# Kernel optimization log

Measured on AMD Instinct MI355X. Metric: run time of the kernel, lower is better.

The kernel has to match this reference:

```python
import jax, jax.numpy as jnp
import numpy as np

SEQ_LEN = 512
PRED_LEN = 96
N_BINS = 5


def setup_inputs() -> dict:
    key = jax.random.key(0)
    k1, k2, k3 = jax.random.split(key, 3)
    x = jax.random.normal(k1, (64, 1024, SEQ_LEN), dtype=jnp.float32)
    # nn.Linear(seq_len, pred_len): weight (pred_len, seq_len), bias (pred_len,)
    W = jax.random.normal(k2, (PRED_LEN, SEQ_LEN), dtype=jnp.float32) / np.sqrt(SEQ_LEN)
    b = jax.random.normal(k3, (PRED_LEN,), dtype=jnp.float32) * 0.01
    return {"x": x, "W": W, "b": b}


def reference(x, W, b):
    # Exact low-pass trend: keep lowest N_BINS rfft bins, zero the rest, invert.
    X = jnp.fft.rfft(x, axis=-1)                      # (B, N, seq_len//2+1) complex
    n_freq = X.shape[-1]
    keep = (jnp.arange(n_freq) < N_BINS)              # low-pass mask
    X_low = jnp.where(keep, X, 0.0)
    trend = jnp.fft.irfft(X_low, n=SEQ_LEN, axis=-1).astype(x.dtype)  # (B, N, seq_len)
    resid = x - trend
    trend_forecast = jnp.einsum('bns,ps->bnp', trend, W) + b          # (B, N, pred_len)
    return (trend_forecast, resid)
```

## Files before the change

kernel.cpp:

```cpp
#include <hip/hip_runtime.h>

#define SEQL 512
#define PREDL 96
#define NB 9
#define WBPAD 12
#define RU 8

typedef float fvec4 __attribute__((ext_vector_type(4)));

__device__ __forceinline__ float wave_sum_bcast(float v) {
    int t;
    t = __builtin_amdgcn_update_dpp(0, __float_as_int(v), 0x111, 0xf, 0xf, true); v += __int_as_float(t);
    t = __builtin_amdgcn_update_dpp(0, __float_as_int(v), 0x112, 0xf, 0xf, true); v += __int_as_float(t);
    t = __builtin_amdgcn_update_dpp(0, __float_as_int(v), 0x114, 0xf, 0xf, true); v += __int_as_float(t);
    t = __builtin_amdgcn_update_dpp(0, __float_as_int(v), 0x118, 0xf, 0xf, true); v += __int_as_float(t);
    t = __builtin_amdgcn_update_dpp(0, __float_as_int(v), 0x142, 0xf, 0xf, true); v += __int_as_float(t);
    t = __builtin_amdgcn_update_dpp(0, __float_as_int(v), 0x143, 0xf, 0xf, true); v += __int_as_float(t);
    return __int_as_float(__builtin_amdgcn_readlane(__float_as_int(v), 63));
}

__global__ void basis_kernel(float* __restrict__ tbl) {
    int s = threadIdx.x;
    if (s >= SEQL) return;
    tbl[0 * SEQL + s] = 1.0f;
    #pragma unroll
    for (int k = 1; k <= 4; ++k) {
        int m = (k * s) & (SEQL - 1);
        float ang = (float)m * (6.283185307179586f / SEQL);
        float sn, cs;
        __sincosf(ang, &sn, &cs);
        tbl[(2 * k - 1) * SEQL + s] = cs;
        tbl[(2 * k    ) * SEQL + s] = sn;
    }
}

__global__ __launch_bounds__(64)
void wb_kernel(const float* __restrict__ W, const float* __restrict__ tbl,
               float* __restrict__ wb) {
    int p = blockIdx.x;
    int lane = threadIdx.x;
    const float* wr = W + (size_t)p * SEQL + lane * 8;
    float4 wa = *(const float4*)(wr);
    float4 wz = *(const float4*)(wr + 4);
    float wv[8] = {wa.x, wa.y, wa.z, wa.w, wz.x, wz.y, wz.z, wz.w};
    #pragma unroll
    for (int j = 0; j < NB; ++j) {
        const float* bj = tbl + j * SEQL + lane * 8;
        float4 b0 = *(const float4*)bj;
        float4 b1 = *(const float4*)(bj + 4);
        float bb[8] = {b0.x, b0.y, b0.z, b0.w, b1.x, b1.y, b1.z, b1.w};
        float acc = 0.f;
        #pragma unroll
        for (int e = 0; e < 8; ++e) acc += wv[e] * bb[e];
        float s = wave_sum_bcast(acc);
        if (lane == 0) wb[p * WBPAD + j] = s;
    }
}

__global__ __launch_bounds__(256, 2)
void detrend_kernel(const float* __restrict__ x, const float* __restrict__ bias,
                    const float* __restrict__ tbl, const float* __restrict__ wb,
                    float* __restrict__ fc, float* __restrict__ resid, int nrows) {
    const int lane = threadIdx.x & 63;
    const int wid  = threadIdx.x >> 6;
    const int gw   = blockIdx.x * (blockDim.x >> 6) + wid;
    const int r0   = gw * RU;
    if (r0 >= nrows) return;

    float4 xl[RU][2];
    #pragma unroll
    for (int u = 0; u < RU; ++u) {
        const float* xr = x + (size_t)(r0 + u) * SEQL + lane * 8;
        xl[u][0] = *(const float4*)xr;
        xl[u][1] = *(const float4*)(xr + 4);
    }

    float bas[NB][8];
    #pragma unroll
    for (int j = 0; j < NB; ++j) {
        const float* bj = tbl + j * SEQL + lane * 8;
        float4 b0 = *(const float4*)bj;
        float4 b1 = *(const float4*)(bj + 4);
        bas[j][0] = b0.x; bas[j][1] = b0.y; bas[j][2] = b0.z; bas[j][3] = b0.w;
        bas[j][4] = b1.x; bas[j][5] = b1.y; bas[j][6] = b1.z; bas[j][7] = b1.w;
    }
    const int p0 = lane;
    const int p1 = 64 + lane;
    float wb0[NB], wb1[NB], bv0, bv1 = 0.f;
    #pragma unroll
    for (int j = 0; j < NB; ++j) wb0[j] = wb[p0 * WBPAD + j];
    bv0 = bias[p0];
    if (lane < 32) {
        #pragma unroll
        for (int j = 0; j < NB; ++j) wb1[j] = wb[p1 * WBPAD + j];
        bv1 = bias[p1];
    }

    #pragma unroll
    for (int u = 0; u < RU; ++u) {
        float xv[8] = {xl[u][0].x, xl[u][0].y, xl[u][0].z, xl[u][0].w,
                       xl[u][1].x, xl[u][1].y, xl[u][1].z, xl[u][1].w};
        float acc[NB];
        #pragma unroll
        for (int j = 0; j < NB; ++j) acc[j] = 0.f;
        #pragma unroll
        for (int e = 0; e < 8; ++e)
            #pragma unroll
            for (int j = 0; j < NB; ++j) acc[j] += xv[e] * bas[j][e];
        acc[0] *= (1.0f / SEQL);
        #pragma unroll
        for (int j = 1; j < NB; ++j) acc[j] *= (2.0f / SEQL);
        float c[NB];
        #pragma unroll
        for (int j = 0; j < NB; ++j) c[j] = wave_sum_bcast(acc[j]);

        float rv[8];
        #pragma unroll
        for (int e = 0; e < 8; ++e) {
            float t = 0.f;
            #pragma unroll
            for (int j = 0; j < NB; ++j) t += c[j] * bas[j][e];
            rv[e] = xv[e] - t;
        }
        float* rr = resid + (size_t)(r0 + u) * SEQL + lane * 8;
        fvec4 v0 = {rv[0], rv[1], rv[2], rv[3]};
        fvec4 v1 = {rv[4], rv[5], rv[6], rv[7]};
        __builtin_nontemporal_store(v0, (fvec4*)rr);
        __builtin_nontemporal_store(v1, (fvec4*)(rr + 4));

        float* fr = fc + (size_t)(r0 + u) * PREDL;
        float f0 = bv0;
        #pragma unroll
        for (int j = 0; j < NB; ++j) f0 += c[j] * wb0[j];
        __builtin_nontemporal_store(f0, fr + p0);
        if (lane < 32) {
            float f1 = bv1;
            #pragma unroll
            for (int j = 0; j < NB; ++j) f1 += c[j] * wb1[j];
            __builtin_nontemporal_store(f1, fr + p1);
        }
    }
}

extern "C" void kernel_launch(void* const* d_in, const int* in_sizes, int n_in,
                              void* d_out, int out_size, void* d_ws, size_t ws_size,
                              hipStream_t stream) {
    const float* x = (const float*)d_in[0];
    const float* W = (const float*)d_in[1];
    const float* b = (const float*)d_in[2];
    float* fc = (float*)d_out;
    const int nrows = in_sizes[0] / SEQL;
    float* resid = fc + (size_t)nrows * PREDL;
    float* tbl = (float*)d_ws;
    float* wb  = tbl + NB * SEQL;

    hipLaunchKernelGGL(basis_kernel, dim3(1), dim3(SEQL), 0, stream, tbl);
    hipLaunchKernelGGL(wb_kernel, dim3(PREDL), dim3(64), 0, stream, W, tbl, wb);
    hipLaunchKernelGGL(detrend_kernel, dim3(2048), dim3(256), 0, stream,
                       x, b, tbl, wb, fc, resid, nrows);
}
```

Baseline: 67.83 us.

## Split detrend into coefficient pass and apply pass with grid-stride loops

Splits the fused detrend kernel into two kernels. The first computes the 9 Fourier coefficients per row and writes them to a workspace buffer. The second re-reads x together with those coefficients to produce the residual and the forecast. Both use persistent grid-stride loops, and the fused fallback also becomes grid-stride with smaller unrolling. This is meant to separate the reduction-heavy phase from the store-heavy phase, at the cost of reading x twice, which adds about 128 MB of extra traffic.

Result: slower. 99.56 us (+46.8%).

```diff
diff --git a/kernel.cpp b/kernel.cpp
--- a/kernel.cpp
+++ b/kernel.cpp
@@ -4,7 +4,9 @@
 #define PREDL 96
 #define NB 9
 #define WBPAD 12
-#define RU 8
+#define RU1 8
+#define RU2 4
+#define RUF 4
 
 typedef float fvec4 __attribute__((ext_vector_type(4)));
 
@@ -57,23 +59,143 @@
     }
 }
 
-__global__ __launch_bounds__(256, 2)
+__global__ __launch_bounds__(256)
+void coef_kernel(const float* __restrict__ x, const float* __restrict__ tbl,
+                 float* __restrict__ cbuf, int nrows) {
+    const int lane = threadIdx.x & 63;
+    const int wid  = threadIdx.x >> 6;
+    const int gw   = blockIdx.x * (blockDim.x >> 6) + wid;
+    const int nw   = gridDim.x * (blockDim.x >> 6);
+
+    float bas[NB][8];
+    #pragma unroll
+    for (int j = 0; j < NB; ++j) {
+        const float* bj = tbl + j * SEQL + lane * 8;
+        float4 b0 = *(const float4*)bj;
+        float4 b1 = *(const float4*)(bj + 4);
+        bas[j][0] = b0.x; bas[j][1] = b0.y; bas[j][2] = b0.z; bas[j][3] = b0.w;
+        bas[j][4] = b1.x; bas[j][5] = b1.y; bas[j][6] = b1.z; bas[j][7] = b1.w;
+    }
+
+    for (int r0 = gw * RU1; r0 < nrows; r0 += nw * RU1) {
+        float4 xl[RU1][2];
+        #pragma unroll
+        for (int u = 0; u < RU1; ++u) {
+            const float* xr = x + (size_t)(r0 + u) * SEQL + lane * 8;
+            xl[u][0] = *(const float4*)xr;
+            xl[u][1] = *(const float4*)(xr + 4);
+        }
+        #pragma unroll
+        for (int u = 0; u < RU1; ++u) {
+            float xv[8] = {xl[u][0].x, xl[u][0].y, xl[u][0].z, xl[u][0].w,
+                           xl[u][1].x, xl[u][1].y, xl[u][1].z, xl[u][1].w};
+            float acc[NB];
+            #pragma unroll
+            for (int j = 0; j < NB; ++j) acc[j] = 0.f;
+            #pragma unroll
+            for (int e = 0; e < 8; ++e)
+                #pragma unroll
+                for (int j = 0; j < NB; ++j) acc[j] += xv[e] * bas[j][e];
+            acc[0] *= (1.0f / SEQL);
+            #pragma unroll
+            for (int j = 1; j < NB; ++j) acc[j] *= (2.0f / SEQL);
+            float c[NB];
+            #pragma unroll
+            for (int j = 0; j < NB; ++j) c[j] = wave_sum_bcast(acc[j]);
+            float v = c[0];
+            #pragma unroll
+            for (int j = 1; j < NB; ++j) v = (lane == j) ? c[j] : v;
+            if (lane < NB) cbuf[(size_t)(r0 + u) * NB + lane] = v;
+        }
+    }
+}
+
+__global__ __launch_bounds__(256)
+void apply_kernel(const float* __restrict__ x, const float* __restrict__ bias,
+                  const float* __restrict__ tbl, const float* __restrict__ wb,
+                  const float* __restrict__ cbuf,
+                  float* __restrict__ fc, float* __restrict__ resid, int nrows) {
+    const int lane = threadIdx.x & 63;
+    const int wid  = threadIdx.x >> 6;
+    const int gw   = blockIdx.x * (blockDim.x >> 6) + wid;
+    const int nw   = gridDim.x * (blockDim.x >> 6);
+
+    float bas[NB][8];
+    #pragma unroll
+    for (int j = 0; j < NB; ++j) {
+        const float* bj = tbl + j * SEQL + lane * 8;
+        float4 b0 = *(const float4*)bj;
+        float4 b1 = *(const float4*)(bj + 4);
+        bas[j][0] = b0.x; bas[j][1] = b0.y; bas[j][2] = b0.z; bas[j][3] = b0.w;
+        bas[j][4] = b1.x; bas[j][5] = b1.y; bas[j][6] = b1.z; bas[j][7] = b1.w;
+    }
+    const int p0 = lane;
+    const int p1 = 64 + lane;
+    float wb0[NB], wb1[NB], bv0, bv1 = 0.f;
+    #pragma unroll
+    for (int j = 0; j < NB; ++j) wb0[j] = wb[p0 * WBPAD + j];
+    bv0 = bias[p0];
+    if (lane < 32) {
+        #pragma unroll
+        for (int j = 0; j < NB; ++j) wb1[j] = wb[p1 * WBPAD + j];
+        bv1 = bias[p1];
+    }
+
+    for (int r0 = gw * RU2; r0 < nrows; r0 += nw * RU2) {
+        float4 xl[RU2][2];
+        #pragma unroll
+        for (int u = 0; u < RU2; ++u) {
+            const float* xr = x + (size_t)(r0 + u) * SEQL + lane * 8;
+            xl[u][0] = *(const float4*)xr;
+            xl[u][1] = *(const float4*)(xr + 4);
+        }
+        float cmy = (lane < RU2 * NB) ? cbuf[(size_t)r0 * NB + lane] : 0.f;
+
+        #pragma unroll
+        for (int u = 0; u < RU2; ++u) {
+            float c[NB];
+            #pragma unroll
+            for (int j = 0; j < NB; ++j) c[j] = __shfl(cmy, u * NB + j, 64);
+
+            float xv[8] = {xl[u][0].x, xl[u][0].y, xl[u][0].z, xl[u][0].w,
+                           xl[u][1].x, xl[u][1].y, xl[u][1].z, xl[u][1].w};
+            float rv[8];
+            #pragma unroll
+            for (int e = 0; e < 8; ++e) {
+                float t = 0.f;
+                #pragma unroll
+                for (int j = 0; j < NB; ++j) t += c[j] * bas[j][e];
+                rv[e] = xv[e] - t;
+            }
+            float* rr = resid + (size_t)(r0 + u) * SEQL + lane * 8;
+            fvec4 v0 = {rv[0], rv[1], rv[2], rv[3]};
+            fvec4 v1 = {rv[4], rv[5], rv[6], rv[7]};
+            __builtin_nontemporal_store(v0, (fvec4*)rr);
+            __builtin_nontemporal_store(v1, (fvec4*)(rr + 4));
+
+            float* fr = fc + (size_t)(r0 + u) * PREDL;
+            float f0 = bv0;
+            #pragma unroll
+            for (int j = 0; j < NB; ++j) f0 += c[j] * wb0[j];
+            __builtin_nontemporal_store(f0, fr + p0);
+            if (lane < 32) {
+                float f1 = bv1;
+                #pragma unroll
+                for (int j = 0; j < NB; ++j) f1 += c[j] * wb1[j];
+                __builtin_nontemporal_store(f1, fr + p1);
+            }
+        }
+    }
+}
+
+__global__ __launch_bounds__(256)
 void detrend_kernel(const float* __restrict__ x, const float* __restrict__ bias,
                     const float* __restrict__ tbl, const float* __restrict__ wb,
                     float* __restrict__ fc, float* __restrict__ resid, int nrows) {
     const int lane = threadIdx.x & 63;
     const int wid  = threadIdx.x >> 6;
     const int gw   = blockIdx.x * (blockDim.x >> 6) + wid;
-    const int r0   = gw * RU;
-    if (r0 >= nrows) return;
-
-    float4 xl[RU][2];
-    #pragma unroll
-    for (int u = 0; u < RU; ++u) {
-        const float* xr = x + (size_t)(r0 + u) * SEQL + lane * 8;
-        xl[u][0] = *(const float4*)xr;
-        xl[u][1] = *(const float4*)(xr + 4);
-    }
+    const int nw   = gridDim.x * (blockDim.x >> 6);
 
     float bas[NB][8];
     #pragma unroll
@@ -96,48 +218,57 @@
         bv1 = bias[p1];
     }
 
-    #pragma unroll
-    for (int u = 0; u < RU; ++u) {
-        float xv[8] = {xl[u][0].x, xl[u][0].y, xl[u][0].z, xl[u][0].w,
-                       xl[u][1].x, xl[u][1].y, xl[u][1].z, xl[u][1].w};
-        float acc[NB];
-        #pragma unroll
-        for (int j = 0; j < NB; ++j) acc[j] = 0.f;
-        #pragma unroll
-        for (int e = 0; e < 8; ++e)
-            #pragma unroll
-            for (int j = 0; j < NB; ++j) acc[j] += xv[e] * bas[j][e];
-        acc[0] *= (1.0f / SEQL);
-        #pragma unroll
-        for (int j = 1; j < NB; ++j) acc[j] *= (2.0f / SEQL);
-        float c[NB];
-        #pragma unroll
-        for (int j = 0; j < NB; ++j) c[j] = wave_sum_bcast(acc[j]);
-
-        float rv[8];
-        #pragma unroll
-        for (int e = 0; e < 8; ++e) {
-            float t = 0.f;
-            #pragma unroll
-            for (int j = 0; j < NB; ++j) t += c[j] * bas[j][e];
-            rv[e] = xv[e] - t;
-        }
-        float* rr = resid + (size_t)(r0 + u) * SEQL + lane * 8;
-        fvec4 v0 = {rv[0], rv[1], rv[2], rv[3]};
-        fvec4 v1 = {rv[4], rv[5], rv[6], rv[7]};
-        __builtin_nontemporal_store(v0, (fvec4*)rr);
-        __builtin_nontemporal_store(v1, (fvec4*)(rr + 4));
-
-        float* fr = fc + (size_t)(r0 + u) * PREDL;
-        float f0 = bv0;
-        #pragma unroll
-        for (int j = 0; j < NB; ++j) f0 += c[j] * wb0[j];
-        __builtin_nontemporal_store(f0, fr + p0);
-        if (lane < 32) {
-            float f1 = bv1;
-            #pragma unroll
-            for (int j = 0; j < NB; ++j) f1 += c[j] * wb1[j];
-            __builtin_nontemporal_store(f1, fr + p1);
+    for (int r0 = gw * RUF; r0 < nrows; r0 += nw * RUF) {
+        float4 xl[RUF][2];
+        #pragma unroll
+        for (int u = 0; u < RUF; ++u) {
+            const float* xr = x + (size_t)(r0 + u) * SEQL + lane * 8;
+            xl[u][0] = *(const float4*)xr;
+            xl[u][1] = *(const float4*)(xr + 4);
+        }
+        #pragma unroll
+        for (int u = 0; u < RUF; ++u) {
+            float xv[8] = {xl[u][0].x, xl[u][0].y, xl[u][0].z, xl[u][0].w,
+                           xl[u][1].x, xl[u][1].y, xl[u][1].z, xl[u][1].w};
+            float acc[NB];
+            #pragma unroll
+            for (int j = 0; j < NB; ++j) acc[j] = 0.f;
+            #pragma unroll
+            for (int e = 0; e < 8; ++e)
+                #pragma unroll
+                for (int j = 0; j < NB; ++j) acc[j] += xv[e] * bas[j][e];
+            acc[0] *= (1.0f / SEQL);
+            #pragma unroll
+            for (int j = 1; j < NB; ++j) acc[j] *= (2.0f / SEQL);
+            float c[NB];
+            #pragma unroll
+            for (int j = 0; j < NB; ++j) c[j] = wave_sum_bcast(acc[j]);
+
+            float rv[8];
+            #pragma unroll
+            for (int e = 0; e < 8; ++e) {
+                float t = 0.f;
+                #pragma unroll
+                for (int j = 0; j < NB; ++j) t += c[j] * bas[j][e];
+                rv[e] = xv[e] - t;
+            }
+            float* rr = resid + (size_t)(r0 + u) * SEQL + lane * 8;
+            fvec4 v0 = {rv[0], rv[1], rv[2], rv[3]};
+            fvec4 v1 = {rv[4], rv[5], rv[6], rv[7]};
+            __builtin_nontemporal_store(v0, (fvec4*)rr);
+            __builtin_nontemporal_store(v1, (fvec4*)(rr + 4));
+
+            float* fr = fc + (size_t)(r0 + u) * PREDL;
+            float f0 = bv0;
+            #pragma unroll
+            for (int j = 0; j < NB; ++j) f0 += c[j] * wb0[j];
+            __builtin_nontemporal_store(f0, fr + p0);
+            if (lane < 32) {
+                float f1 = bv1;
+                #pragma unroll
+                for (int j = 0; j < NB; ++j) f1 += c[j] * wb1[j];
+                __builtin_nontemporal_store(f1, fr + p1);
+            }
         }
     }
 }
@@ -153,9 +284,19 @@
     float* resid = fc + (size_t)nrows * PREDL;
     float* tbl = (float*)d_ws;
     float* wb  = tbl + NB * SEQL;
+    float* cbuf = wb + PREDL * WBPAD;
+    const size_t ws_need = ((size_t)NB * SEQL + PREDL * WBPAD + (size_t)nrows * NB) * 4;
 
     hipLaunchKernelGGL(basis_kernel, dim3(1), dim3(SEQL), 0, stream, tbl);
     hipLaunchKernelGGL(wb_kernel, dim3(PREDL), dim3(64), 0, stream, W, tbl, wb);
-    hipLaunchKernelGGL(detrend_kernel, dim3(2048), dim3(256), 0, stream,
-                       x, b, tbl, wb, fc, resid, nrows);
-}
+
+    if (ws_size >= ws_need) {
+        hipLaunchKernelGGL(coef_kernel, dim3(1024), dim3(256), 0, stream,
+                           x, tbl, cbuf, nrows);
+        hipLaunchKernelGGL(apply_kernel, dim3(1024), dim3(256), 0, stream,
+                           x, b, tbl, wb, cbuf, fc, resid, nrows);
+    } else {
+        hipLaunchKernelGGL(detrend_kernel, dim3(2048), dim3(256), 0, stream,
+                           x, b, tbl, wb, fc, resid, nrows);
+    }
+}
```

## Persistent double-buffered detrend loop with half-period symmetry basis folding

Applied to the files above, without the earlier changes.

Turns the detrend kernel into a grid-stride persistent loop over half as many blocks, prefetching the next group of rows into a second register buffer while the current group is processed. Each lane now reads elements s and s+256 and uses the parity of the low-frequency basis under a half-period shift, so it keeps only half the basis table in registers and does roughly half the projection multiplies. Rows per step drop from 8 to 4 and the occupancy hint in the launch bounds is removed. The aim is to overlap memory loads with the reduction work and to cut register pressure and ALU work, but the deeper loop logic and fewer blocks may leave bandwidth unused.

Result: faster. 60.47 us (-10.8%).

```diff
diff --git a/kernel.cpp b/kernel.cpp
--- a/kernel.cpp
+++ b/kernel.cpp
@@ -4,7 +4,7 @@
 #define PREDL 96
 #define NB 9
 #define WBPAD 12
-#define RU 8
+#define RU 4
 
 typedef float fvec4 __attribute__((ext_vector_type(4)));
 
@@ -57,32 +57,21 @@
     }
 }
 
-__global__ __launch_bounds__(256, 2)
+__global__ __launch_bounds__(256)
 void detrend_kernel(const float* __restrict__ x, const float* __restrict__ bias,
                     const float* __restrict__ tbl, const float* __restrict__ wb,
                     float* __restrict__ fc, float* __restrict__ resid, int nrows) {
     const int lane = threadIdx.x & 63;
     const int wid  = threadIdx.x >> 6;
     const int gw   = blockIdx.x * (blockDim.x >> 6) + wid;
-    const int r0   = gw * RU;
-    if (r0 >= nrows) return;
-
-    float4 xl[RU][2];
-    #pragma unroll
-    for (int u = 0; u < RU; ++u) {
-        const float* xr = x + (size_t)(r0 + u) * SEQL + lane * 8;
-        xl[u][0] = *(const float4*)xr;
-        xl[u][1] = *(const float4*)(xr + 4);
-    }
-
-    float bas[NB][8];
-    #pragma unroll
-    for (int j = 0; j < NB; ++j) {
-        const float* bj = tbl + j * SEQL + lane * 8;
-        float4 b0 = *(const float4*)bj;
-        float4 b1 = *(const float4*)(bj + 4);
+    const int nw   = gridDim.x * (blockDim.x >> 6);
+    const int step = nw * RU;
+
+    float bas[NB][4];
+    #pragma unroll
+    for (int j = 1; j < NB; ++j) {
+        float4 b0 = *(const float4*)(tbl + j * SEQL + lane * 4);
         bas[j][0] = b0.x; bas[j][1] = b0.y; bas[j][2] = b0.z; bas[j][3] = b0.w;
-        bas[j][4] = b1.x; bas[j][5] = b1.y; bas[j][6] = b1.z; bas[j][7] = b1.w;
     }
     const int p0 = lane;
     const int p1 = 64 + lane;
@@ -96,50 +85,103 @@
         bv1 = bias[p1];
     }
 
+    float4 bufA0[RU], bufA1[RU];
+    float4 bufB0[RU], bufB1[RU];
+
+    int r = gw * RU;
+    if (r >= nrows) return;
+
     #pragma unroll
     for (int u = 0; u < RU; ++u) {
-        float xv[8] = {xl[u][0].x, xl[u][0].y, xl[u][0].z, xl[u][0].w,
-                       xl[u][1].x, xl[u][1].y, xl[u][1].z, xl[u][1].w};
-        float acc[NB];
-        #pragma unroll
-        for (int j = 0; j < NB; ++j) acc[j] = 0.f;
-        #pragma unroll
-        for (int e = 0; e < 8; ++e)
+        const float* xr = x + (size_t)(r + u) * SEQL + lane * 4;
+        bufA0[u] = *(const float4*)xr;
+        bufB0[u] = *(const float4*)(xr + 256);
+    }
+
+    #define PROCESS(BA, BB, RR)                                                     \
+    {                                                                               \
+        _Pragma("unroll")                                                           \
+        for (int u = 0; u < RU; ++u) {                                              \
+            float ue[4], ve[4];                                                     \
+            ue[0]=BA[u].x+BB[u].x; ue[1]=BA[u].y+BB[u].y;                           \
+            ue[2]=BA[u].z+BB[u].z; ue[3]=BA[u].w+BB[u].w;                           \
+            ve[0]=BA[u].x-BB[u].x; ve[1]=BA[u].y-BB[u].y;                           \
+            ve[2]=BA[u].z-BB[u].z; ve[3]=BA[u].w-BB[u].w;                           \
+            float acc[NB];                                                          \
+            acc[0] = (ue[0]+ue[1]) + (ue[2]+ue[3]);                                 \
+            acc[1]=0.f; acc[2]=0.f; acc[5]=0.f; acc[6]=0.f;       \
+            acc[3]=0.f; acc[4]=0.f; acc[7]=0.f; acc[8]=0.f;      \
+            _Pragma("unroll")                                                       \
+            for (int e = 0; e < 4; ++e) {                                           \
+                acc[1] += ve[e]*bas[1][e]; acc[2] += ve[e]*bas[2][e];               \
+                acc[5] += ve[e]*bas[5][e]; acc[6] += ve[e]*bas[6][e];               \
+                acc[3] += ue[e]*bas[3][e]; acc[4] += ue[e]*bas[4][e];               \
+                acc[7] += ue[e]*bas[7][e]; acc[8] += ue[e]*bas[8][e];               \
+            }                                                                       \
+            acc[0] *= (1.0f / SEQL);                                                \
+            _Pragma("unroll")                                                       \
+            for (int j = 1; j < NB; ++j) acc[j] *= (2.0f / SEQL);                   \
+            float c[NB];                                                            \
+            _Pragma("unroll")                                                       \
+            for (int j = 0; j < NB; ++j) c[j] = wave_sum_bcast(acc[j]);             \
+            float r0v[4], r1v[4];                                                   \
+            _Pragma("unroll")                                                       \
+            for (int e = 0; e < 4; ++e) {                                           \
+                float te = c[0] + c[3]*bas[3][e] + c[4]*bas[4][e]                   \
+                                + c[7]*bas[7][e] + c[8]*bas[8][e];                  \
+                float to = c[1]*bas[1][e] + c[2]*bas[2][e]                          \
+                         + c[5]*bas[5][e] + c[6]*bas[6][e];                         \
+                float av = (e==0)?BA[u].x:(e==1)?BA[u].y:(e==2)?BA[u].z:BA[u].w;    \
+                float bv = (e==0)?BB[u].x:(e==1)?BB[u].y:(e==2)?BB[u].z:BB[u].w;    \
+                r0v[e] = av - (te + to);                                            \
+                r1v[e] = bv - (te - to);                                            \
+            }                                                                       \
+            float* rr = resid + (size_t)((RR) + u) * SEQL + lane * 4;               \
+            fvec4 s0v = {r0v[0], r0v[1], r0v[2], r0v[3]};                           \
+            fvec4 s1v = {r1v[0], r1v[1], r1v[2], r1v[3]};                           \
+            __builtin_nontemporal_store(s0v, (fvec4*)rr);                           \
+            __builtin_nontemporal_store(s1v, (fvec4*)(rr + 256));                   \
+            float* fr = fc + (size_t)((RR) + u) * PREDL;                            \
+            float f0 = bv0;                                                         \
+            _Pragma("unroll")                                                       \
+            for (int j = 0; j < NB; ++j) f0 += c[j] * wb0[j];                       \
+            __builtin_nontemporal_store(f0, fr + p0);                               \
+            if (lane < 32) {                                                        \
+                float f1 = bv1;                                                     \
+                _Pragma("unroll")                                                   \
+                for (int j = 0; j < NB; ++j) f1 += c[j] * wb1[j];                   \
+                __builtin_nontemporal_store(f1, fr + p1);                           \
+            }                                                                       \
+        }                                                                           \
+    }
+
+    while (true) {
+        int r1 = r + step;
+        if (r1 < nrows) {
             #pragma unroll
-            for (int j = 0; j < NB; ++j) acc[j] += xv[e] * bas[j][e];
-        acc[0] *= (1.0f / SEQL);
-        #pragma unroll
-        for (int j = 1; j < NB; ++j) acc[j] *= (2.0f / SEQL);
-        float c[NB];
-        #pragma unroll
-        for (int j = 0; j < NB; ++j) c[j] = wave_sum_bcast(acc[j]);
-
-        float rv[8];
-        #pragma unroll
-        for (int e = 0; e < 8; ++e) {
-            float t = 0.f;
+            for (int u = 0; u < RU; ++u) {
+                const float* xr = x + (size_t)(r1 + u) * SEQL + lane * 4;
+                bufA1[u] = *(const float4*)xr;
+                bufB1[u] = *(const float4*)(xr + 256);
+            }
+        }
+        PROCESS(bufA0, bufB0, r);
+        if (r1 >= nrows) break;
+
+        int r2 = r1 + step;
+        if (r2 < nrows) {
             #pragma unroll
-            for (int j = 0; j < NB; ++j) t += c[j] * bas[j][e];
-            rv[e] = xv[e] - t;
+            for (int u = 0; u < RU; ++u) {
+                const float* xr = x + (size_t)(r2 + u) * SEQL + lane * 4;
+                bufA0[u] = *(const float4*)xr;
+                bufB0[u] = *(const float4*)(xr + 256);
+            }
         }
-        float* rr = resid + (size_t)(r0 + u) * SEQL + lane * 8;
-        fvec4 v0 = {rv[0], rv[1], rv[2], rv[3]};
-        fvec4 v1 = {rv[4], rv[5], rv[6], rv[7]};
-        __builtin_nontemporal_store(v0, (fvec4*)rr);
-        __builtin_nontemporal_store(v1, (fvec4*)(rr + 4));
-
-        float* fr = fc + (size_t)(r0 + u) * PREDL;
-        float f0 = bv0;
-        #pragma unroll
-        for (int j = 0; j < NB; ++j) f0 += c[j] * wb0[j];
-        __builtin_nontemporal_store(f0, fr + p0);
-        if (lane < 32) {
-            float f1 = bv1;
-            #pragma unroll
-            for (int j = 0; j < NB; ++j) f1 += c[j] * wb1[j];
-            __builtin_nontemporal_store(f1, fr + p1);
-        }
-    }
+        PROCESS(bufA1, bufB1, r1);
+        if (r2 >= nrows) break;
+        r = r2;
+    }
+    #undef PROCESS
 }
 
 extern "C" void kernel_launch(void* const* d_in, const int* in_sizes, int n_in,
@@ -156,6 +198,6 @@
 
     hipLaunchKernelGGL(basis_kernel, dim3(1), dim3(SEQL), 0, stream, tbl);
     hipLaunchKernelGGL(wb_kernel, dim3(PREDL), dim3(64), 0, stream, W, tbl, wb);
-    hipLaunchKernelGGL(detrend_kernel, dim3(2048), dim3(256), 0, stream,
+    hipLaunchKernelGGL(detrend_kernel, dim3(1024), dim3(256), 0, stream,
                        x, b, tbl, wb, fc, resid, nrows);
 }
```
